# Performance work log

Measured on AMD Instinct MI355X. Metric: run time of the kernel, lower is better.

The kernel has to match this reference:

```python
import math
import jax, jax.numpy as jnp
import numpy as np

B, L, U, D, H, VOCAB = 8, 512, 24, 1024, 16, 54945
T = 3 * U
CSK = 1024
BN_EPS = 1e-5


def _heads(x, H):
    b, t, dm = x.shape
    d = dm // H
    return x.reshape(b, t, H, d).transpose(0, 2, 1, 3)  # [B,H,T,d]


def _masked_attn(x, mask, edge_type, Wq, bq, Wk, bk, Wv, bv, rel_table, n_heads):
    # Faithful to MaskedSelfAttention.forward with edge_type: at query row i the
    # query/key layers have accumulated sum_{j<=i} rel_layer_j added (in-place += in torch).
    b, t, dm = x.shape
    d = dm // n_heads
    Q = _heads(x @ Wq + bq, n_heads)
    K = _heads(x @ Wk + bk, n_heads)
    V = _heads(x @ Wv + bv, n_heads)
    # rel_table[edge_type]: [B, i(rel row), p(pos), D] -> [B, i, H, p, d]
    R = rel_table[edge_type].reshape(b, t, t, n_heads, d).transpose(0, 1, 3, 2, 4)
    S = jnp.cumsum(R, axis=1)  # inclusive prefix sum over relation-row index i
    # S_diag[b,h,i,d] = S[b,i,h,i,d] : accumulated rel at query position i
    S_diag = jnp.moveaxis(jnp.diagonal(S, axis1=1, axis2=3), -1, 2)  # [B,H,T,d]
    A = Q + S_diag  # effective query rows
    # scores[b,h,i,k] = A[b,h,i] . (K[b,h,k] + S[b,i,h,k])
    scores = (jnp.einsum('bhid,bhkd->bhik', A, K)
              + jnp.einsum('bhid,bihkd->bhik', A, S)) / math.sqrt(d)
    scores = jnp.where(mask[:, None, :, :] == 0, -1e9, scores)
    probs = jax.nn.softmax(scores, axis=-1)  # dropout omitted (eval mode)
    ctx = jnp.einsum('bhik,bhkd->bhid', probs, V)
    return ctx.transpose(0, 2, 1, 3).reshape(b, t, dm)


def setup_inputs() -> dict:
    key = jax.random.key(0)
    ks = jax.random.split(key, 30)
    p = lambda k, shape: (jax.random.normal(k, shape, jnp.float32) * 0.02)
    rel_table = p(ks[8], (8, D)).at[0].set(0.0)  # padding_idx=0
    inp = {
        'hidden_states': jax.random.normal(ks[0], (B, L, D), jnp.float32),
        'emo_csk': jax.random.normal(ks[1], (B, U, CSK), jnp.float32),
        'Wq': p(ks[2], (D, D)), 'bq': jnp.zeros((D,), jnp.float32),
        'Wk': p(ks[3], (D, D)), 'bk': jnp.zeros((D,), jnp.float32),
        'Wv': p(ks[4], (D, D)), 'bv': jnp.zeros((D,), jnp.float32),
        'rel_table': rel_table,
        'fusion_W': p(ks[5], (2 * D, D)), 'fusion_b': jnp.zeros((D,), jnp.float32),
        'bn_gamma': jnp.ones((CSK,), jnp.float32), 'bn_beta': jnp.zeros((CSK,), jnp.float32),
        'bn_mean': p(ks[6], (CSK,)), 'bn_var': jnp.ones((CSK,), jnp.float32),
        'csk_W': p(ks[7], (CSK, D)), 'csk_b': jnp.zeros((D,), jnp.float32),
        'emo_W': p(ks[9], (D, 6)), 'emo_b': jnp.zeros((6,), jnp.float32),
        'str_W': p(ks[10], (D, 8)), 'str_b': jnp.zeros((8,), jnp.float32),
        'bow_W': p(ks[11], (D, VOCAB)),
        'trans_cls_index': jnp.sort(jax.random.randint(ks[12], (B, U), 2, L), axis=-1),
        'trans_graph': jax.random.randint(ks[13], (B, T, T), 0, 2, jnp.int32),
        'inter_graph': jax.random.randint(ks[14], (B, T, T), 0, 2, jnp.int32),
        'trans_edge_type': jax.random.randint(ks[15], (B, T, T), 0, 8, jnp.int32),
        'inter_edge_type': jax.random.randint(ks[16], (B, T, T), 0, 8, jnp.int32),
    }
    return inp


def reference(hidden_states, emo_csk, Wq, bq, Wk, bk, Wv, bv, rel_table,
              fusion_W, fusion_b, bn_gamma, bn_beta, bn_mean, bn_var,
              csk_W, csk_b, emo_W, emo_b, str_W, str_b, bow_W,
              trans_cls_index, trans_graph, inter_graph,
              trans_edge_type, inter_edge_type):
    b, l, dm = hidden_states.shape
    u = trans_cls_index.shape[1]
    # per-conversation CLS gather (all indices valid: text_len == U)
    cls_emb = jnp.take_along_axis(hidden_states, trans_cls_index[:, :, None], axis=1)  # [B,U,D]
    sem_cls_embs = cls_emb
    # BatchNorm1d (eval: running stats) + linear 1024->D
    csk_norm = (emo_csk - bn_mean) / jnp.sqrt(bn_var + BN_EPS) * bn_gamma + bn_beta
    csk_proj = csk_norm @ csk_W + csk_b  # [B,U,D]
    # _prepare_for_transition: [cls, cls, cls(+csk if not last)] per utterance -> T=3U
    trans_in = jnp.repeat(cls_emb, 3, axis=1)  # [B,3U,D]
    not_last = (jnp.arange(u) < u - 1).astype(csk_proj.dtype)[None, :, None]
    trans_in = trans_in.at[:, 2::3, :].add(csk_proj * not_last)
    attn = lambda x, m, e: _masked_attn(x, m, e, Wq, bq, Wk, bk, Wv, bv, rel_table, H)
    trans_out = attn(trans_in, trans_graph, trans_edge_type)
    inter_out = attn(trans_out, inter_graph, inter_edge_type)
    gate = jax.nn.sigmoid(jnp.concatenate([trans_out, inter_out], axis=-1) @ fusion_W + fusion_b)
    outputs = (1.0 - gate) * inter_out + gate * trans_out
    sem_trans = outputs[:, 0::3]
    stra_trans = outputs[:, 1::3]
    emo_trans = outputs[:, 2::3]
    last_stra_state = stra_trans[:, u - 1]
    delta = sem_trans - sem_cls_embs
    last_delta = delta[:, u - 1]
    bow_logits = delta @ bow_W
    emotion_logits = emo_trans @ emo_W + emo_b
    strategy_logits = stra_trans @ str_W + str_b
    return (last_stra_state, emo_trans, last_delta, sem_cls_embs,
            strategy_logits, emotion_logits, bow_logits)
```

## Files before the change

kernel.cpp:

```cpp
#include <hip/hip_runtime.h>
#include <math.h>

#define BB 8
#define LL 512
#define UU 24
#define DD 1024
#define HH 16
#define DH 64
#define TT 72
#define CSKN 1024
#define NVOCAB 54945

typedef __attribute__((ext_vector_type(8))) short bf16x8;
typedef __attribute__((ext_vector_type(4))) float f32x4;

__device__ inline unsigned short f2b(float x) {
    unsigned u = __float_as_uint(x);
    unsigned r = u + 0x7FFFu + ((u >> 16) & 1u);
    return (unsigned short)(r >> 16);
}
__device__ inline unsigned pack2(float lo, float hi) {
    return (unsigned)f2b(lo) | ((unsigned)f2b(hi) << 16);
}
__device__ inline void dec8(uint2 c, float* cr) {
    cr[0] = (float)( c.x        & 0xff); cr[1] = (float)((c.x >>  8) & 0xff);
    cr[2] = (float)((c.x >> 16) & 0xff); cr[3] = (float)((c.x >> 24) & 0xff);
    cr[4] = (float)( c.y        & 0xff); cr[5] = (float)((c.y >>  8) & 0xff);
    cr[6] = (float)((c.y >> 16) & 0xff); cr[7] = (float)((c.y >> 24) & 0xff);
}

__global__ __launch_bounds__(256) void k_gather_cls(const float* __restrict__ hidden,
        const int* __restrict__ idx, float* __restrict__ sem_cls, float* __restrict__ trans_in)
{
    int bid = blockIdx.x; int b = bid / UU, u = bid % UU;
    int row = idx[b*UU + u];
    const float* src = hidden + ((size_t)(b*LL + row))*DD;
    float* d0 = trans_in + ((size_t)(b*TT + 3*u))*DD;
    float* sc = sem_cls + ((size_t)(b*UU + u))*DD;
    for (int d = threadIdx.x; d < DD; d += 256) {
        float v = src[d];
        sc[d] = v;
        d0[d] = v; d0[DD + d] = v; d0[2*DD + d] = v;
    }
}

__global__ void k_bn(const float* __restrict__ x, const float* __restrict__ g,
                     const float* __restrict__ be, const float* __restrict__ mu,
                     const float* __restrict__ var, float* __restrict__ y, int n)
{
    int i = blockIdx.x*256 + threadIdx.x;
    if (i >= n) return;
    int c = i % CSKN;
    y[i] = (x[i] - mu[c]) * (1.0f/sqrtf(var[c] + 1e-5f)) * g[c] + be[c];
}

template<int EPI>
__global__ __launch_bounds__(256) void mm64(
        const float* __restrict__ A1, const float* __restrict__ A2, int K1,
        const float* __restrict__ Bm, const float* __restrict__ bias,
        const float* __restrict__ ep1, const float* __restrict__ ep2,
        float* __restrict__ C, int N, int K)
{
    __shared__ __align__(16) unsigned short As[2][64][40];
    __shared__ __align__(16) unsigned short Bs[2][64][40];
    int tid = threadIdx.x;
    int wave = tid >> 6, lane = tid & 63;
    int l16 = lane & 15, g = lane >> 4;
    int wm = wave & 1, wn = wave >> 1;
    int row0 = blockIdx.y * 64, col0 = blockIdx.x * 64;

    int ar = tid >> 2, akq = (tid & 3) * 8;
    int bj0 = (tid & 31) * 2, bk0 = (tid >> 5) * 2;
    float4 a0, a1;
    float2 q00, q01, q10, q11;

    auto loadT = [&](int k0) {
        int kk = k0 + akq;
        const float* src = (kk < K1) ? A1 + (size_t)(row0+ar)*K1 + kk
                                     : A2 + (size_t)(row0+ar)*(K-K1) + (kk-K1);
        a0 = *(const float4*)src; a1 = *(const float4*)(src+4);
        const float* bs0 = Bm + (size_t)(k0 + bk0)*N + col0 + bj0;
        q00 = *(const float2*)bs0;       q01 = *(const float2*)(bs0 + N);
        const float* bs1 = bs0 + (size_t)16*N;
        q10 = *(const float2*)bs1;       q11 = *(const float2*)(bs1 + N);
    };
    auto storeT = [&](int buf) {
        unsigned* da = (unsigned*)&As[buf][ar][akq];
        da[0] = pack2(a0.x, a0.y); da[1] = pack2(a0.z, a0.w);
        da[2] = pack2(a1.x, a1.y); da[3] = pack2(a1.z, a1.w);
        *(unsigned*)&Bs[buf][bj0  ][bk0]    = pack2(q00.x, q01.x);
        *(unsigned*)&Bs[buf][bj0+1][bk0]    = pack2(q00.y, q01.y);
        *(unsigned*)&Bs[buf][bj0  ][bk0+16] = pack2(q10.x, q11.x);
        *(unsigned*)&Bs[buf][bj0+1][bk0+16] = pack2(q10.y, q11.y);
    };

    f32x4 acc[2][2] = {};
    loadT(0); storeT(0);
    __syncthreads();
    int nt = K / 32;
    for (int t = 0; t < nt; ++t) {
        int cur = t & 1;
        if (t + 1 < nt) loadT((t+1)*32);
        bf16x8 af[2], bfr[2];
        #pragma unroll
        for (int mf = 0; mf < 2; ++mf) af[mf] = *(const bf16x8*)&As[cur][wm*32 + mf*16 + l16][g*8];
        #pragma unroll
        for (int nf = 0; nf < 2; ++nf) bfr[nf] = *(const bf16x8*)&Bs[cur][wn*32 + nf*16 + l16][g*8];
        #pragma unroll
        for (int mf = 0; mf < 2; ++mf)
            #pragma unroll
            for (int nf = 0; nf < 2; ++nf)
                acc[mf][nf] = __builtin_amdgcn_mfma_f32_16x16x32_bf16(af[mf], bfr[nf], acc[mf][nf], 0, 0, 0);
        if (t + 1 < nt) storeT(cur ^ 1);
        __syncthreads();
    }
    #pragma unroll
    for (int mf = 0; mf < 2; ++mf)
        #pragma unroll
        for (int nf = 0; nf < 2; ++nf) {
            int cc = col0 + wn*32 + nf*16 + l16;
            float bv = bias[cc];
            #pragma unroll
            for (int r = 0; r < 4; ++r) {
                int rr = row0 + wm*32 + mf*16 + g*4 + r;
                float v = acc[mf][nf][r] + bv;
                if (EPI == 3) {
                    float gg = 1.0f/(1.0f + __expf(-v));
                    float tv = ep1[(size_t)rr*N + cc];
                    float iv = ep2[(size_t)rr*N + cc];
                    C[(size_t)rr*N + cc] = gg*tv + (1.0f - gg)*iv;
                } else {
                    int bq = rr / UU, uq = rr % UU;
                    if (uq < UU-1) {
                        float* dst = &C[((size_t)(bq*TT + 3*uq + 2))*DD + cc];
                        *dst += v;
                    }
                }
            }
        }
}

__global__ __launch_bounds__(256) void mm_qkv(
        const float* __restrict__ x,
        const float* __restrict__ W0, const float* __restrict__ W1, const float* __restrict__ W2,
        const float* __restrict__ v0, const float* __restrict__ v1, const float* __restrict__ v2,
        float* __restrict__ C0, float* __restrict__ C1, float* __restrict__ C2)
{
    __shared__ __align__(16) unsigned short As[2][64][40];
    __shared__ __align__(16) unsigned short Bs[2][128][40];
    int which = blockIdx.x >> 3;
    int col0 = (blockIdx.x & 7) * 128;
    int row0 = blockIdx.y * 64;
    const float* W  = (which == 0) ? W0 : (which == 1) ? W1 : W2;
    const float* bb = (which == 0) ? v0 : (which == 1) ? v1 : v2;
    float*       C  = (which == 0) ? C0 : (which == 1) ? C1 : C2;
    int tid = threadIdx.x;
    int wave = tid >> 6, lane = tid & 63;
    int l16 = lane & 15, g = lane >> 4;
    int wm = wave & 1, wn = wave >> 1;

    int ar = tid >> 2, akq = (tid & 3) * 8;
    int bj0 = (tid & 63) * 2, ks = tid >> 6;
    float4 a0, a1;
    float2 b0[4], b1[4];

    auto loadT = [&](int k0) {
        const float* src = x + (size_t)(row0+ar)*DD + k0 + akq;
        a0 = *(const float4*)src; a1 = *(const float4*)(src+4);
        #pragma unroll
        for (int s = 0; s < 4; ++s) {
            int kb = (ks + 4*s)*2;
            const float* bp = W + (size_t)(k0 + kb)*DD + col0 + bj0;
            b0[s] = *(const float2*)bp;
            b1[s] = *(const float2*)(bp + DD);
        }
    };
    auto storeT = [&](int buf) {
        unsigned* da = (unsigned*)&As[buf][ar][akq];
        da[0] = pack2(a0.x, a0.y); da[1] = pack2(a0.z, a0.w);
        da[2] = pack2(a1.x, a1.y); da[3] = pack2(a1.z, a1.w);
        #pragma unroll
        for (int s = 0; s < 4; ++s) {
            int kb = (ks + 4*s)*2;
            *(unsigned*)&Bs[buf][bj0  ][kb] = pack2(b0[s].x, b1[s].x);
            *(unsigned*)&Bs[buf][bj0+1][kb] = pack2(b0[s].y, b1[s].y);
        }
    };

    f32x4 acc[2][4] = {};
    loadT(0); storeT(0);
    __syncthreads();
    for (int t = 0; t < 32; ++t) {
        int cur = t & 1;
        if (t < 31) loadT((t+1)*32);
        bf16x8 af[2], bfr[4];
        #pragma unroll
        for (int mf = 0; mf < 2; ++mf) af[mf] = *(const bf16x8*)&As[cur][wm*32 + mf*16 + l16][g*8];
        #pragma unroll
        for (int nf = 0; nf < 4; ++nf) bfr[nf] = *(const bf16x8*)&Bs[cur][wn*64 + nf*16 + l16][g*8];
        #pragma unroll
        for (int mf = 0; mf < 2; ++mf)
            #pragma unroll
            for (int nf = 0; nf < 4; ++nf)
                acc[mf][nf] = __builtin_amdgcn_mfma_f32_16x16x32_bf16(af[mf], bfr[nf], acc[mf][nf], 0, 0, 0);
        if (t < 31) storeT(cur ^ 1);
        __syncthreads();
    }
    #pragma unroll
    for (int mf = 0; mf < 2; ++mf)
        #pragma unroll
        for (int nf = 0; nf < 4; ++nf) {
            int cc = col0 + wn*64 + nf*16 + l16;
            float bv = bb[cc];
            #pragma unroll
            for (int r = 0; r < 4; ++r) {
                int rr = row0 + wm*32 + mf*16 + g*4 + r;
                C[(size_t)rr*DD + cc] = acc[mf][nf][r] + bv;
            }
        }
}

__global__ __launch_bounds__(256) void mm_bow(
        const unsigned short* __restrict__ Ab, const float* __restrict__ Bm,
        float* __restrict__ C)
{
    __shared__ __align__(16) unsigned short A_lds[2][192][40];
    const int N = NVOCAB;
    int tid = threadIdx.x;
    int lane = tid & 63, wave = tid >> 6;
    int l16 = lane & 15, g = lane >> 4;
    int col = blockIdx.x * 64 + wave * 16 + l16;
    int colc = (col < N) ? col : (N - 1);
    const float* bbase = Bm + (size_t)(g * 8) * N + colc;

    int r0 = tid >> 2,          q0 = (tid & 3) * 8;
    int r1 = (tid + 256) >> 2,  q1 = ((tid + 256) & 3) * 8;
    int r2 = (tid + 512) >> 2,  q2 = ((tid + 512) & 3) * 8;
    int4 ra0, ra1, ra2;
    auto loadA = [&](int k0) {
        ra0 = *(const int4*)(Ab + (size_t)r0 * DD + k0 + q0);
        ra1 = *(const int4*)(Ab + (size_t)r1 * DD + k0 + q1);
        ra2 = *(const int4*)(Ab + (size_t)r2 * DD + k0 + q2);
    };
    auto writeA = [&](int buf) {
        *(int4*)&A_lds[buf][r0][q0] = ra0;
        *(int4*)&A_lds[buf][r1][q1] = ra1;
        *(int4*)&A_lds[buf][r2][q2] = ra2;
    };

    f32x4 acc[12] = {};
    float bA[8], bB[8];

#define LOADB(dst, t_) { const float* bp = bbase + (size_t)(t_) * 32 * N;      \
        _Pragma("unroll") for (int j = 0; j < 8; ++j) dst[j] = bp[(size_t)j * N]; }
#define PACKB(fr, sv) { _Pragma("unroll") for (int j = 0; j < 8; ++j)          \
        ((unsigned short*)&fr)[j] = f2b(sv[j]); }
#define MFMA12(buf, fr) { _Pragma("unroll") for (int mf = 0; mf < 12; ++mf) {  \
        bf16x8 af = *(const bf16x8*)&A_lds[buf][mf * 16 + l16][g * 8];         \
        acc[mf] = __builtin_amdgcn_mfma_f32_16x16x32_bf16(af, fr, acc[mf], 0, 0, 0); } }

    LOADB(bA, 0); LOADB(bB, 1);
    loadA(0); writeA(0);
    loadA(32);
    __syncthreads();
    for (int t = 0; t < 32; t += 2) {
        bf16x8 fr;
        PACKB(fr, bA);
        if (t + 2 < 32) LOADB(bA, t + 2);
        MFMA12(0, fr);
        if (t + 1 < 32) writeA(1);
        if (t + 2 < 32) loadA((t + 2) * 32);
        __syncthreads();
        PACKB(fr, bB);
        if (t + 3 < 32) LOADB(bB, t + 3);
        MFMA12(1, fr);
        if (t + 2 < 32) writeA(0);
        if (t + 3 < 32) loadA((t + 3) * 32);
        __syncthreads();
    }
#undef LOADB
#undef PACKB
#undef MFMA12
    if (col < N) {
        #pragma unroll
        for (int mf = 0; mf < 12; ++mf)
            #pragma unroll
            for (int r = 0; r < 4; ++r)
                C[(size_t)(mf * 16 + g * 4 + r) * N + col] = acc[mf][r];
    }
}

__global__ __launch_bounds__(256) void k_cnt(const int* __restrict__ et, uint2* __restrict__ cnt)
{
    __shared__ unsigned char e_sh[TT*TT];
    int b = blockIdx.x, tid = threadIdx.x;
    for (int idx = tid; idx < (TT*TT)/4; idx += 256) {
        int4 v = ((const int4*)(et + (size_t)b*TT*TT))[idx];
        unsigned pk = (unsigned)v.x | ((unsigned)v.y << 8) | ((unsigned)v.z << 16) | ((unsigned)v.w << 24);
        *(unsigned*)&e_sh[idx*4] = pk;
    }
    __syncthreads();
    int k = tid;
    if (k < TT) {
        unsigned lo = 0, hi = 0;
        for (int i = 0; i < TT; ++i) {
            int r = e_sh[i*TT + k];
            if (r < 4) lo += 1u << (8*r); else hi += 1u << (8*(r-4));
            cnt[((size_t)b*TT + i)*TT + k] = make_uint2(lo, hi);
        }
    }
}

__global__ __launch_bounds__(512) void k_attn(const float* __restrict__ Qb,
        const float* __restrict__ Kg, const float* __restrict__ Vg,
        const uint2* __restrict__ cnt, const float* __restrict__ rel,
        const int* __restrict__ mask, float* __restrict__ out)
{
    int bid = blockIdx.x;
    int is = bid & 1;
    int h  = (bid >> 1) & (HH-1);
    int b  = bid >> 5;
    __shared__ float K_sh[DH][TT+1];
    __shared__ float V_sh[TT][DH+4];
    __shared__ float rel_sh[8][DH];
    __shared__ float a_row[8][DH];
    __shared__ float p_row[8][TT];
    int tid = threadIdx.x;
    int lane = tid & 63, w = tid >> 6;

    for (int idx = tid; idx < TT*16; idx += 512) {
        int r = idx >> 4, q4 = (idx & 15) * 4;
        size_t goff = ((size_t)(b*TT + r))*DD + h*DH + q4;
        float4 kv = *(const float4*)&Kg[goff];
        K_sh[q4  ][r] = kv.x; K_sh[q4+1][r] = kv.y;
        K_sh[q4+2][r] = kv.z; K_sh[q4+3][r] = kv.w;
        float4 vv = *(const float4*)&Vg[goff];
        *(float4*)&V_sh[r][q4] = vv;
    }
    if (tid < 128) {
        int r = tid >> 4, q4 = (tid & 15) * 4;
        *(float4*)&rel_sh[r][q4] = *(const float4*)&rel[r*DD + h*DH + q4];
    }
    __syncthreads();

    for (int ii = w; ii < TT/2; ii += 8) {
        int i = is*(TT/2) + ii;
        size_t rowoff = (size_t)(b*TT + i);
        float q = Qb[rowoff*DD + h*DH + lane];
        float crd[8]; dec8(cnt[rowoff*TT + i], crd);
        float a = q;
        #pragma unroll
        for (int r = 0; r < 8; ++r) a += crd[r]*rel_sh[r][lane];
        a_row[w][lane] = a;
        float arr[8];
        #pragma unroll
        for (int r = 0; r < 8; ++r) {
            float pr = a * rel_sh[r][lane];
            #pragma unroll
            for (int off = 32; off; off >>= 1) pr += __shfl_xor(pr, off);
            arr[r] = pr;
        }
        float s1;
        {
            int t = lane;
            float s = 0.0f;
            #pragma unroll
            for (int d0 = 0; d0 < DH; d0 += 4) {
                float4 av = *(const float4*)&a_row[w][d0];
                s += av.x*K_sh[d0][t] + av.y*K_sh[d0+1][t]
                   + av.z*K_sh[d0+2][t] + av.w*K_sh[d0+3][t];
            }
            float cr2[8]; dec8(cnt[rowoff*TT + t], cr2);
            float s2v = cr2[0]*arr[0] + cr2[1]*arr[1] + cr2[2]*arr[2] + cr2[3]*arr[3]
                      + cr2[4]*arr[4] + cr2[5]*arr[5] + cr2[6]*arr[6] + cr2[7]*arr[7];
            int m = mask[rowoff*TT + t];
            s1 = (m == 0) ? -1e9f : (s + s2v)*0.125f;
        }
        float s2 = -1e30f;
        if (lane < TT - DH) {
            int t = DH + lane;
            float s = 0.0f;
            #pragma unroll
            for (int d0 = 0; d0 < DH; d0 += 4) {
                float4 av = *(const float4*)&a_row[w][d0];
                s += av.x*K_sh[d0][t] + av.y*K_sh[d0+1][t]
                   + av.z*K_sh[d0+2][t] + av.w*K_sh[d0+3][t];
            }
            float cr2[8]; dec8(cnt[rowoff*TT + t], cr2);
            float s2v = cr2[0]*arr[0] + cr2[1]*arr[1] + cr2[2]*arr[2] + cr2[3]*arr[3]
                      + cr2[4]*arr[4] + cr2[5]*arr[5] + cr2[6]*arr[6] + cr2[7]*arr[7];
            int m = mask[rowoff*TT + t];
            s2 = (m == 0) ? -1e9f : (s + s2v)*0.125f;
        }
        float mx = fmaxf(s1, s2);
        #pragma unroll
        for (int off = 32; off; off >>= 1) mx = fmaxf(mx, __shfl_xor(mx, off));
        float e1 = __expf(s1 - mx);
        float e2 = (lane < TT - DH) ? __expf(s2 - mx) : 0.0f;
        float sm = e1 + e2;
        #pragma unroll
        for (int off = 32; off; off >>= 1) sm += __shfl_xor(sm, off);
        float inv = 1.0f / sm;
        p_row[w][lane] = e1 * inv;
        if (lane < TT - DH) p_row[w][DH + lane] = e2 * inv;
        float o = 0.0f;
        #pragma unroll 8
        for (int t = 0; t < TT; ++t) o += p_row[w][t] * V_sh[t][lane];
        out[rowoff*DD + h*DH + lane] = o;
    }
}

__global__ __launch_bounds__(256) void k_finlog(const float* __restrict__ outs,
        const float* __restrict__ sem_cls,
        const float* __restrict__ strW, const float* __restrict__ strB,
        const float* __restrict__ emoW, const float* __restrict__ emoB,
        float* __restrict__ o_last_stra, float* __restrict__ o_emo,
        float* __restrict__ o_last_delta, float* __restrict__ o_str,
        float* __restrict__ o_emo_log, unsigned short* __restrict__ deltaB)
{
    __shared__ float part[14][16];
    int bid = blockIdx.x; int b = bid / UU, u = bid % UU;
    const float* sem = outs + ((size_t)(b*TT + 3*u))*DD;
    const float* st  = sem + DD;
    const float* em  = st + DD;
    const float* sc  = sem_cls + ((size_t)(b*UU + u))*DD;
    unsigned short* de = deltaB + ((size_t)(b*UU + u))*DD;
    float* oe = o_emo + ((size_t)(b*UU + u))*DD;
    int t = threadIdx.x;
    for (int d = t; d < DD; d += 256) {
        float dl = sem[d] - sc[d];
        de[d] = f2b(dl); oe[d] = em[d];
        if (u == UU-1) { o_last_stra[b*DD + d] = st[d]; o_last_delta[b*DD + d] = dl; }
    }
    if (t < 224) {
        int o = t >> 4, c = t & 15;
        float s = 0.0f;
        if (o < 8) {
            for (int d = c*64; d < c*64 + 64; ++d) s += st[d]*strW[d*8 + o];
        } else {
            int j = o - 8;
            for (int d = c*64; d < c*64 + 64; ++d) s += em[d]*emoW[d*6 + j];
        }
        part[o][c] = s;
    }
    __syncthreads();
    if (t < 14) {
        float s = 0.0f;
        #pragma unroll
        for (int c2 = 0; c2 < 16; ++c2) s += part[t][c2];
        if (t < 8) o_str[(b*UU + u)*8 + t] = s + strB[t];
        else       o_emo_log[(b*UU + u)*6 + (t-8)] = s + emoB[t-8];
    }
}

extern "C" void kernel_launch(void* const* d_in, const int* in_sizes, int n_in,
                              void* d_out, int out_size, void* d_ws, size_t ws_size,
                              hipStream_t stream)
{
    const float* hidden  = (const float*)d_in[0];
    const float* emo_csk = (const float*)d_in[1];
    const float* Wq  = (const float*)d_in[2];
    const float* bq  = (const float*)d_in[3];
    const float* Wk  = (const float*)d_in[4];
    const float* bk  = (const float*)d_in[5];
    const float* Wv  = (const float*)d_in[6];
    const float* bv  = (const float*)d_in[7];
    const float* rel = (const float*)d_in[8];
    const float* fusW = (const float*)d_in[9];
    const float* fusB = (const float*)d_in[10];
    const float* bng = (const float*)d_in[11];
    const float* bnb = (const float*)d_in[12];
    const float* bnm = (const float*)d_in[13];
    const float* bnv = (const float*)d_in[14];
    const float* cskW = (const float*)d_in[15];
    const float* cskB = (const float*)d_in[16];
    const float* emoW = (const float*)d_in[17];
    const float* emoB = (const float*)d_in[18];
    const float* strW = (const float*)d_in[19];
    const float* strB = (const float*)d_in[20];
    const float* bowW = (const float*)d_in[21];
    const int* clsIdx = (const int*)d_in[22];
    const int* tGraph = (const int*)d_in[23];
    const int* iGraph = (const int*)d_in[24];
    const int* tEdge  = (const int*)d_in[25];
    const int* iEdge  = (const int*)d_in[26];

    float* out = (float*)d_out;
    float* o_last_stra  = out;
    float* o_emo_trans  = out + 8192;
    float* o_last_delta = out + 204800;
    float* o_sem_cls    = out + 212992;
    float* o_str_log    = out + 409600;
    float* o_emo_log    = out + 411136;
    float* o_bow        = out + 412288;

    float* ws = (float*)d_ws;
    const int SZ_BTD = BB*TT*DD;
    const int SZ_BUD = BB*UU*DD;
    float* trans_in  = ws;
    float* Qb        = trans_in + SZ_BTD;
    float* Kb        = Qb + SZ_BTD;
    float* Vb        = Kb + SZ_BTD;
    float* trans_out = Vb + SZ_BTD;
    float* inter_out = trans_out + SZ_BTD;
    float* outsB     = inter_out + SZ_BTD;
    float* csk_norm  = outsB + SZ_BTD;
    float* cnt_f     = csk_norm + SZ_BUD;
    uint2* cntb      = (uint2*)cnt_f;
    unsigned short* deltaB = (unsigned short*)(cnt_f + BB*TT*TT*2);

    k_gather_cls<<<dim3(BB*UU), dim3(256), 0, stream>>>(hidden, clsIdx, o_sem_cls, trans_in);
    int nbn = BB*UU*CSKN;
    k_bn<<<dim3((nbn+255)/256), dim3(256), 0, stream>>>(emo_csk, bng, bnb, bnm, bnv, csk_norm, nbn);
    mm64<4><<<dim3(16, 3), dim3(256), 0, stream>>>(csk_norm, nullptr, CSKN, cskW, cskB,
            nullptr, nullptr, trans_in, DD, CSKN);

    auto attention = [&](const float* x, const int* graph, const int* edge, float* ctx_out) {
        mm_qkv<<<dim3(24, (BB*TT)/64), dim3(256), 0, stream>>>(x, Wq, Wk, Wv, bq, bk, bv, Qb, Kb, Vb);
        k_cnt<<<dim3(BB), dim3(256), 0, stream>>>(edge, cntb);
        k_attn<<<dim3(BB*HH*2), dim3(512), 0, stream>>>(Qb, Kb, Vb, cntb, rel, graph, ctx_out);
    };
    attention(trans_in, tGraph, tEdge, trans_out);
    attention(trans_out, iGraph, iEdge, inter_out);

    mm64<3><<<dim3(16, (BB*TT)/64), dim3(256), 0, stream>>>(trans_out, inter_out, DD, fusW, fusB,
            trans_out, inter_out, outsB, DD, 2*DD);

    k_finlog<<<dim3(BB*UU), dim3(256), 0, stream>>>(outsB, o_sem_cls, strW, strB, emoW, emoB,
            o_last_stra, o_emo_trans, o_last_delta, o_str_log, o_emo_log, deltaB);

    mm_bow<<<dim3((NVOCAB+63)/64), dim3(256), 0, stream>>>(deltaB, bowW, o_bow);
}
```

Measured before the change: 327.8 us.

## Load bow A fragments directly from global, drop LDS staging and barriers

The bow-logits GEMM kernel no longer stages the 192x32 bf16 A tile through double-buffered shared memory with __syncthreads. Each wave now reads its A fragments straight from global (cache-resident, since A is small and shared by all blocks). The B prefetch depth goes from 2 to 4 register sets to hide more global latency. This removes LDS writes and block barriers but adds redundant per-wave global loads of A and more registers.

```diff
diff --git a/kernel.cpp b/kernel.cpp
--- a/kernel.cpp
+++ b/kernel.cpp
@@ -224,7 +224,6 @@
         const unsigned short* __restrict__ Ab, const float* __restrict__ Bm,
         float* __restrict__ C)
 {
-    __shared__ __align__(16) unsigned short A_lds[2][192][40];
     const int N = NVOCAB;
     int tid = threadIdx.x;
     int lane = tid & 63, wave = tid >> 6;
@@ -232,55 +231,31 @@
     int col = blockIdx.x * 64 + wave * 16 + l16;
     int colc = (col < N) ? col : (N - 1);
     const float* bbase = Bm + (size_t)(g * 8) * N + colc;
-
-    int r0 = tid >> 2,          q0 = (tid & 3) * 8;
-    int r1 = (tid + 256) >> 2,  q1 = ((tid + 256) & 3) * 8;
-    int r2 = (tid + 512) >> 2,  q2 = ((tid + 512) & 3) * 8;
-    int4 ra0, ra1, ra2;
-    auto loadA = [&](int k0) {
-        ra0 = *(const int4*)(Ab + (size_t)r0 * DD + k0 + q0);
-        ra1 = *(const int4*)(Ab + (size_t)r1 * DD + k0 + q1);
-        ra2 = *(const int4*)(Ab + (size_t)r2 * DD + k0 + q2);
-    };
-    auto writeA = [&](int buf) {
-        *(int4*)&A_lds[buf][r0][q0] = ra0;
-        *(int4*)&A_lds[buf][r1][q1] = ra1;
-        *(int4*)&A_lds[buf][r2][q2] = ra2;
-    };
+    const unsigned short* abase = Ab + (size_t)l16 * DD + g * 8;
 
     f32x4 acc[12] = {};
-    float bA[8], bB[8];
+    float bA[8], bB[8], bC[8], bD[8];
 
 #define LOADB(dst, t_) { const float* bp = bbase + (size_t)(t_) * 32 * N;      \
         _Pragma("unroll") for (int j = 0; j < 8; ++j) dst[j] = bp[(size_t)j * N]; }
-#define PACKB(fr, sv) { _Pragma("unroll") for (int j = 0; j < 8; ++j)          \
-        ((unsigned short*)&fr)[j] = f2b(sv[j]); }
-#define MFMA12(buf, fr) { _Pragma("unroll") for (int mf = 0; mf < 12; ++mf) {  \
-        bf16x8 af = *(const bf16x8*)&A_lds[buf][mf * 16 + l16][g * 8];         \
-        acc[mf] = __builtin_amdgcn_mfma_f32_16x16x32_bf16(af, fr, acc[mf], 0, 0, 0); } }
-
-    LOADB(bA, 0); LOADB(bB, 1);
-    loadA(0); writeA(0);
-    loadA(32);
-    __syncthreads();
-    for (int t = 0; t < 32; t += 2) {
-        bf16x8 fr;
-        PACKB(fr, bA);
-        if (t + 2 < 32) LOADB(bA, t + 2);
-        MFMA12(0, fr);
-        if (t + 1 < 32) writeA(1);
-        if (t + 2 < 32) loadA((t + 2) * 32);
-        __syncthreads();
-        PACKB(fr, bB);
-        if (t + 3 < 32) LOADB(bB, t + 3);
-        MFMA12(1, fr);
-        if (t + 2 < 32) writeA(0);
-        if (t + 3 < 32) loadA((t + 3) * 32);
-        __syncthreads();
+#define STEP(bset, t_) {                                                       \
+        bf16x8 fr;                                                             \
+        _Pragma("unroll") for (int j = 0; j < 8; ++j)                          \
+            ((unsigned short*)&fr)[j] = f2b(bset[j]);                          \
+        if ((t_) + 4 < 32) LOADB(bset, (t_) + 4);                              \
+        _Pragma("unroll") for (int mf = 0; mf < 12; ++mf) {                    \
+            bf16x8 af = *(const bf16x8*)(abase + (size_t)(mf*16)*DD + (t_)*32);\
+            acc[mf] = __builtin_amdgcn_mfma_f32_16x16x32_bf16(af, fr, acc[mf], 0, 0, 0); } }
+
+    LOADB(bA, 0); LOADB(bB, 1); LOADB(bC, 2); LOADB(bD, 3);
+    for (int t = 0; t < 32; t += 4) {
+        STEP(bA, t);
+        STEP(bB, t + 1);
+        STEP(bC, t + 2);
+        STEP(bD, t + 3);
     }
 #undef LOADB
-#undef PACKB
-#undef MFMA12
+#undef STEP
     if (col < N) {
         #pragma unroll
         for (int mf = 0; mf < 12; ++mf)
```

Result: slower. 464.9 us (+41.8%).
